# Kernel optimization log

Measured on AMD Instinct MI355X. Metric: run time of the kernel, lower is better.

## Reference

```python
import jax, jax.numpy as jnp
import numpy as np
import math

# Derived from BilateralDenoiser.set_influence(1.0):
#   sigma = max(2*influence, 1e-4) = 2.0; window N = 2*ceil(2.5*sigma)+1 = 11
SIGMA = 2.0
NORMAL_POWER = 128.0  # normal-similarity exponent in the CUDA kernel
EPS = 1e-4


def setup_inputs() -> dict:
    key = jax.random.key(0)
    k1, k2, k3 = jax.random.split(key, 3)
    B, H, W = 4, 1024, 1024
    col = jax.random.uniform(k1, (B, H, W, 3), jnp.float32)
    nrm = jax.random.normal(k2, (B, H, W, 3), jnp.float32)
    nrm = nrm / jnp.linalg.norm(nrm, axis=-1, keepdims=True)  # unit normals
    zdz = jax.random.uniform(k3, (B, H, W, 2), jnp.float32)   # (depth, |d depth|)
    return {"col": col, "nrm": nrm, "zdz": zdz}


def _denoise(col, nrm, zdz):
    # col/nrm: [B,H,W,3]; zdz: [B,H,W,2]
    B, H, W, _ = col.shape
    variance = SIGMA * SIGMA
    rad = int(math.ceil(SIGMA * 2.5))  # 5 -> 11x11 window
    yy = jnp.arange(H)
    xx = jnp.arange(W)
    c_z = zdz[..., 0]   # center depth
    c_dz = zdz[..., 1]  # center depth-gradient magnitude
    accum_c = jnp.zeros((B, H, W, 3), col.dtype)
    accum_w = jnp.zeros((B, H, W), col.dtype)
    for dy in range(-rad, rad + 1):
        my = (yy + dy >= 0) & (yy + dy < H)
        for dx in range(-rad, rad + 1):
            mx = (xx + dx >= 0) & (xx + dx < W)
            valid = (my[:, None] & mx[None, :]).astype(col.dtype)  # skip OOB taps
            # tap value at pixel (y+dy, x+dx), vectorized over the whole image
            t_col = jnp.roll(col, (-dy, -dx), axis=(1, 2))
            t_nrm = jnp.roll(nrm, (-dy, -dx), axis=(1, 2))
            t_z = jnp.roll(c_z, (-dy, -dx), axis=(1, 2))
            dist_sqr = float(dx * dx + dy * dy)
            dist = math.sqrt(dist_sqr)
            w_xy = math.exp(-dist_sqr / (2.0 * variance))  # spatial Gaussian (scalar)
            w_n = jnp.clip(jnp.sum(t_nrm * nrm, axis=-1), 0.0, 1.0) ** NORMAL_POWER
            w_d = jnp.exp(-jnp.abs(t_z - c_z) / jnp.maximum(c_dz * dist, EPS))
            w = w_xy * w_n * w_d * valid  # [B,H,W]
            accum_c = accum_c + t_col * w[..., None]
            accum_w = accum_w + w
    # module forward: col_w[..., 0:3] / col_w[..., 3:4]
    return accum_c / accum_w[..., None]


def reference(col, nrm, zdz):
    return _denoise(col, nrm, zdz)
```

## Files before the change

### kernel.cpp

```cpp
#include <hip/hip_runtime.h>

#define RAD 5
#define BX 32
#define BY 16
#define PX 2
#define NTX 16
#define TW (BX + 2*RAD)
#define TH (BY + 2*RAD)
#define TWP (TW + 1)

#define LOG2E 1.44269504f
#define CLAMP2 14426.950f
#define PC1 184.664963f
#define PC2 -92.3324814f
#define PC3 61.5549876f

__device__ __constant__ const float kLG[6] = {
    0.0f, -0.18033688f, -0.72134752f, -1.62303192f, -2.88539008f, -4.50842200f};
__device__ __constant__ const float kINVD[6][6] = {
    {1e30f,       1.0f,        0.5f,        0.33333333f, 0.25f,       0.2f},
    {1.0f,        0.70710678f, 0.44721360f, 0.31622777f, 0.24253563f, 0.19611614f},
    {0.5f,        0.44721360f, 0.35355339f, 0.27735010f, 0.22360680f, 0.18569534f},
    {0.33333333f, 0.31622777f, 0.27735010f, 0.23570226f, 0.2f,        0.17149859f},
    {0.25f,       0.24253563f, 0.22360680f, 0.2f,        0.17677670f, 0.15617376f},
    {0.2f,        0.19611614f, 0.18569534f, 0.17149859f, 0.15617376f, 0.14142136f}};

__global__ __launch_bounds__(256, 4) void bilateral_kernel(
    const float* __restrict__ col, const float* __restrict__ nrm,
    const float* __restrict__ zdz, float* __restrict__ out,
    int H, int W) {
  __shared__ float4 s_w[TH][TWP];
  __shared__ uint2  s_c[TH][TWP];

  const int bx = blockIdx.x, by = blockIdx.y, bz = blockIdx.z;
  const int gx0 = bx * BX - RAD;
  const int gy0 = by * BY - RAD;
  const int tid = threadIdx.x;
  const int plane = bz * H * W;

  for (int i = tid; i < TH * TW; i += 256) {
    const int r = i / TW;
    const int c = i - r * TW;
    const int gy = gy0 + r, gx = gx0 + c;
    float4 wv = make_float4(0.f, 0.f, 0.f, 0.f);
    uint2 cv = make_uint2(0u, 0u);
    if ((unsigned)gy < (unsigned)H && (unsigned)gx < (unsigned)W) {
      const int pix = plane + gy * W + gx;
      const float* np_ = nrm + pix * 3;
      wv.x = np_[0]; wv.y = np_[1]; wv.z = np_[2];
      wv.w = zdz[pix * 2];
      const float* cp = col + pix * 3;
      const unsigned ur = (__float_as_uint(cp[0]) + 0x8000u) >> 16;
      const unsigned ug = (__float_as_uint(cp[1]) + 0x8000u) & 0xffff0000u;
      const unsigned ub = (__float_as_uint(cp[2]) + 0x8000u) & 0xffff0000u;
      cv.x = ur | ug;
      cv.y = ub;
    }
    s_w[r][c] = wv;
    s_c[r][c] = cv;
  }
  __syncthreads();

  const int tx = tid & (NTX - 1);
  const int ty = tid >> 4;
  const int ly = ty + RAD;
  const int lxbase = tx * PX;
  const int oy = by * BY + ty;
  const int ox0 = bx * BX + tx * PX;

  float cnx[PX], cny[PX], cnz[PX], czv[PX], rc2[PX];
  float accx[PX], accy[PX], accz[PX], accw[PX];
#pragma unroll
  for (int p = 0; p < PX; ++p) {
    const float4 wv = s_w[ly][lxbase + RAD + p];
    cnx[p] = wv.x; cny[p] = wv.y; cnz[p] = wv.z;
    czv[p] = wv.w;
    const float cdz = zdz[(plane + oy * W + ox0 + p) * 2 + 1];
    rc2[p] = LOG2E / cdz;
    accx[p] = 0.f; accy[p] = 0.f; accz[p] = 0.f; accw[p] = 0.f;
  }

#pragma unroll 1
  for (int dy = -RAD; dy <= RAD; ++dy) {
    const int ady = dy < 0 ? -dy : dy;
    const float kg_ady = kLG[ady];
    const float* irow = kINVD[ady];
    float sA[6];
    float il2s[6][PX];
#pragma unroll
    for (int j = 0; j < 6; ++j) {
      sA[j] = kLG[j] + kg_ady;
      const float iv = irow[j];
#pragma unroll
      for (int p = 0; p < PX; ++p) il2s[j][p] = fminf(rc2[p] * iv, CLAMP2);
    }

    const float4* rowW = &s_w[ly + dy][lxbase];
    const uint2* rowC = &s_c[ly + dy][lxbase];

#pragma unroll
    for (int u = 0; u < 2 * RAD + PX; ++u) {
      const float4 wv = rowW[u];
      const uint2 cv = rowC[u];
      const float tr = __uint_as_float(cv.x << 16);
      const float tg = __uint_as_float(cv.x & 0xffff0000u);
      const float tb = __uint_as_float(cv.y);
#pragma unroll
      for (int p = 0; p < PX; ++p) {
        const int dx = u - RAD - p;
        if (dx < -RAD || dx > RAD) continue;
        const int adx = dx < 0 ? -dx : dx;
        const float d1 = fmaf(wv.x, cnx[p],
                         fmaf(wv.y, cny[p], fmaf(wv.z, cnz[p], -1.0f)));
        const float f = fmaxf(d1, -1.0f);
        const float dz = wv.w - czv[p];
        const float ct = fmaf(-fabsf(dz), il2s[adx][p], sA[adx]);
        const float t1 = fmaf(f, PC3, PC2);
        const float t2 = fmaf(f, t1, PC1);
        const float e = fmaf(f, t2, ct);
        const float w = __builtin_amdgcn_exp2f(e);
        accx[p] = fmaf(tr, w, accx[p]);
        accy[p] = fmaf(tg, w, accy[p]);
        accz[p] = fmaf(tb, w, accz[p]);
        accw[p] += w;
      }
    }
  }

#pragma unroll
  for (int p = 0; p < PX; ++p) {
    const int pix = plane + oy * W + ox0 + p;
    const float inv = 1.0f / accw[p];
    float* op = out + pix * 3;
    op[0] = accx[p] * inv;
    op[1] = accy[p] * inv;
    op[2] = accz[p] * inv;
  }
}

extern "C" void kernel_launch(void* const* d_in, const int* in_sizes, int n_in,
                              void* d_out, int out_size, void* d_ws, size_t ws_size,
                              hipStream_t stream) {
  const float* col = (const float*)d_in[0];
  const float* nrm = (const float*)d_in[1];
  const float* zdz = (const float*)d_in[2];
  float* out = (float*)d_out;
  const int H = 1024, W = 1024;
  const int B = in_sizes[0] / (3 * H * W);
  dim3 grid(W / BX, H / BY, B);
  bilateral_kernel<<<grid, dim3(256), 0, stream>>>(col, nrm, zdz, out, H, W);
}
```

Before: 316.3 us.

## Compute 2x2 outputs per thread with even/odd-split shared tile and larger blocks

Each thread now computes a 2x2 pixel patch instead of 1x2. Each loaded tap row feeds two output rows, which cuts shared-memory reads per tap. The shared tile is stored with even and odd columns split into halves, so adjacent threads read consecutive entries without padding and avoid bank conflicts. Blocks grow to 64x32 pixels with 512 threads, and the spatial-weight sums move to a precomputed 2D constant table with a sentinel row for out-of-range offsets. The cost is more registers per thread, which may reduce occupancy under the 512x4 launch bound.

```diff
diff --git a/kernel.cpp b/kernel.cpp
--- a/kernel.cpp
+++ b/kernel.cpp
@@ -1,13 +1,16 @@
 #include <hip/hip_runtime.h>
 
 #define RAD 5
-#define BX 32
-#define BY 16
+#define BX 64
+#define BY 32
 #define PX 2
-#define NTX 16
+#define PY 2
+#define NTX 32
+#define NTY 16
+#define NT 512
 #define TW (BX + 2*RAD)
 #define TH (BY + 2*RAD)
-#define TWP (TW + 1)
+#define HALF (TW/2)
 
 #define LOG2E 1.44269504f
 #define CLAMP2 14426.950f
@@ -15,22 +18,29 @@
 #define PC2 -92.3324814f
 #define PC3 61.5549876f
 
-__device__ __constant__ const float kLG[6] = {
-    0.0f, -0.18033688f, -0.72134752f, -1.62303192f, -2.88539008f, -4.50842200f};
-__device__ __constant__ const float kINVD[6][6] = {
+__device__ __constant__ const float kSA[7][6] = {
+    {0.0f, -0.18033688f, -0.72134752f, -1.62303192f, -2.88539008f, -4.50842200f},
+    {-0.18033688f, -0.36067376f, -0.90168440f, -1.80336880f, -3.06572696f, -4.68875888f},
+    {-0.72134752f, -0.90168440f, -1.44269504f, -2.34437944f, -3.60673760f, -5.22976952f},
+    {-1.62303192f, -1.80336880f, -2.34437944f, -3.24606384f, -4.50842200f, -6.13145392f},
+    {-2.88539008f, -3.06572696f, -3.60673760f, -4.50842200f, -5.77078016f, -7.39381208f},
+    {-4.50842200f, -4.68875888f, -5.22976952f, -6.13145392f, -7.39381208f, -9.01684400f},
+    {-1e30f, -1e30f, -1e30f, -1e30f, -1e30f, -1e30f}};
+__device__ __constant__ const float kINVD[7][6] = {
     {1e30f,       1.0f,        0.5f,        0.33333333f, 0.25f,       0.2f},
     {1.0f,        0.70710678f, 0.44721360f, 0.31622777f, 0.24253563f, 0.19611614f},
     {0.5f,        0.44721360f, 0.35355339f, 0.27735010f, 0.22360680f, 0.18569534f},
     {0.33333333f, 0.31622777f, 0.27735010f, 0.23570226f, 0.2f,        0.17149859f},
     {0.25f,       0.24253563f, 0.22360680f, 0.2f,        0.17677670f, 0.15617376f},
-    {0.2f,        0.19611614f, 0.18569534f, 0.17149859f, 0.15617376f, 0.14142136f}};
+    {0.2f,        0.19611614f, 0.18569534f, 0.17149859f, 0.15617376f, 0.14142136f},
+    {0.16666667f, 0.16439899f, 0.15811388f, 0.14907120f, 0.13867505f, 0.12803688f}};
 
-__global__ __launch_bounds__(256, 4) void bilateral_kernel(
+__global__ __launch_bounds__(512, 4) void bilateral_kernel(
     const float* __restrict__ col, const float* __restrict__ nrm,
     const float* __restrict__ zdz, float* __restrict__ out,
     int H, int W) {
-  __shared__ float4 s_w[TH][TWP];
-  __shared__ uint2  s_c[TH][TWP];
+  __shared__ float4 s_w[TH][TW];
+  __shared__ uint2  s_c[TH][TW];
 
   const int bx = blockIdx.x, by = blockIdx.y, bz = blockIdx.z;
   const int gx0 = bx * BX - RAD;
@@ -38,9 +48,10 @@
   const int tid = threadIdx.x;
   const int plane = bz * H * W;
 
-  for (int i = tid; i < TH * TW; i += 256) {
+  for (int i = tid; i < TH * TW; i += NT) {
     const int r = i / TW;
     const int c = i - r * TW;
+    const int pc = (c >> 1) + (c & 1) * HALF;
     const int gy = gy0 + r, gx = gx0 + c;
     float4 wv = make_float4(0.f, 0.f, 0.f, 0.f);
     uint2 cv = make_uint2(0u, 0u);
@@ -56,85 +67,114 @@
       cv.x = ur | ug;
       cv.y = ub;
     }
-    s_w[r][c] = wv;
-    s_c[r][c] = cv;
+    s_w[r][pc] = wv;
+    s_c[r][pc] = cv;
   }
   __syncthreads();
 
   const int tx = tid & (NTX - 1);
-  const int ty = tid >> 4;
-  const int ly = ty + RAD;
-  const int lxbase = tx * PX;
-  const int oy = by * BY + ty;
+  const int ty = tid >> 5;
+  const int oy0 = by * BY + ty * PY;
   const int ox0 = bx * BX + tx * PX;
 
-  float cnx[PX], cny[PX], cnz[PX], czv[PX], rc2[PX];
-  float accx[PX], accy[PX], accz[PX], accw[PX];
+  float cnx[2][2], cny[2][2], cnz[2][2], czv[2][2], rc2[2][2];
+  float accx[2][2], accy[2][2], accz[2][2], accw[2][2];
 #pragma unroll
-  for (int p = 0; p < PX; ++p) {
-    const float4 wv = s_w[ly][lxbase + RAD + p];
-    cnx[p] = wv.x; cny[p] = wv.y; cnz[p] = wv.z;
-    czv[p] = wv.w;
-    const float cdz = zdz[(plane + oy * W + ox0 + p) * 2 + 1];
-    rc2[p] = LOG2E / cdz;
-    accx[p] = 0.f; accy[p] = 0.f; accz[p] = 0.f; accw[p] = 0.f;
+  for (int q = 0; q < 2; ++q) {
+#pragma unroll
+    for (int p = 0; p < 2; ++p) {
+      const int c = tx * PX + RAD + p;
+      const int pc = (c >> 1) + (c & 1) * HALF;
+      const float4 wv = s_w[ty * PY + RAD + q][pc];
+      cnx[q][p] = wv.x; cny[q][p] = wv.y; cnz[q][p] = wv.z;
+      czv[q][p] = wv.w;
+      const float cdz = zdz[(plane + (oy0 + q) * W + ox0 + p) * 2 + 1];
+      rc2[q][p] = LOG2E / cdz;
+      accx[q][p] = 0.f; accy[q][p] = 0.f; accz[q][p] = 0.f; accw[q][p] = 0.f;
+    }
   }
 
 #pragma unroll 1
-  for (int dy = -RAD; dy <= RAD; ++dy) {
-    const int ady = dy < 0 ? -dy : dy;
-    const float kg_ady = kLG[ady];
-    const float* irow = kINVD[ady];
-    float sA[6];
-    float il2s[6][PX];
+  for (int trow = 0; trow < 2 * RAD + PY; ++trow) {
+    const int dy0 = trow - RAD;
+    const int ady0 = dy0 < 0 ? -dy0 : dy0;
+    const int dy1 = trow - RAD - 1;
+    const int ady1 = dy1 < 0 ? -dy1 : dy1;
+    const float* __restrict__ sa0 = kSA[ady0];
+    const float* __restrict__ sa1 = kSA[ady1];
+    const float* __restrict__ iv0 = kINVD[ady0];
+    const float* __restrict__ iv1 = kINVD[ady1];
+    float il20[6][2], il21[6][2];
 #pragma unroll
     for (int j = 0; j < 6; ++j) {
-      sA[j] = kLG[j] + kg_ady;
-      const float iv = irow[j];
+      const float v0 = iv0[j], v1 = iv1[j];
 #pragma unroll
-      for (int p = 0; p < PX; ++p) il2s[j][p] = fminf(rc2[p] * iv, CLAMP2);
+      for (int p = 0; p < 2; ++p) {
+        il20[j][p] = fminf(rc2[0][p] * v0, CLAMP2);
+        il21[j][p] = fminf(rc2[1][p] * v1, CLAMP2);
+      }
     }
-
-    const float4* rowW = &s_w[ly + dy][lxbase];
-    const uint2* rowC = &s_c[ly + dy][lxbase];
+    const float4* __restrict__ rowW = &s_w[ty * PY + trow][tx];
+    const uint2* __restrict__ rowC = &s_c[ty * PY + trow][tx];
 
 #pragma unroll
     for (int u = 0; u < 2 * RAD + PX; ++u) {
-      const float4 wv = rowW[u];
-      const uint2 cv = rowC[u];
-      const float tr = __uint_as_float(cv.x << 16);
-      const float tg = __uint_as_float(cv.x & 0xffff0000u);
-      const float tb = __uint_as_float(cv.y);
+      const int off = (u >> 1) + (u & 1) * HALF;
+      const float4 wv = rowW[off];
+      const uint2 cv = rowC[off];
+      const float tcr = __uint_as_float(cv.x << 16);
+      const float tcg = __uint_as_float(cv.x & 0xffff0000u);
+      const float tcb = __uint_as_float(cv.y);
 #pragma unroll
-      for (int p = 0; p < PX; ++p) {
+      for (int p = 0; p < 2; ++p) {
         const int dx = u - RAD - p;
         if (dx < -RAD || dx > RAD) continue;
         const int adx = dx < 0 ? -dx : dx;
-        const float d1 = fmaf(wv.x, cnx[p],
-                         fmaf(wv.y, cny[p], fmaf(wv.z, cnz[p], -1.0f)));
-        const float f = fmaxf(d1, -1.0f);
-        const float dz = wv.w - czv[p];
-        const float ct = fmaf(-fabsf(dz), il2s[adx][p], sA[adx]);
-        const float t1 = fmaf(f, PC3, PC2);
-        const float t2 = fmaf(f, t1, PC1);
-        const float e = fmaf(f, t2, ct);
-        const float w = __builtin_amdgcn_exp2f(e);
-        accx[p] = fmaf(tr, w, accx[p]);
-        accy[p] = fmaf(tg, w, accy[p]);
-        accz[p] = fmaf(tb, w, accz[p]);
-        accw[p] += w;
+        {
+          const float d1 = fmaf(wv.x, cnx[0][p],
+                           fmaf(wv.y, cny[0][p], fmaf(wv.z, cnz[0][p], -1.0f)));
+          const float f = fmaxf(d1, -1.0f);
+          const float dzv = wv.w - czv[0][p];
+          const float ct = fmaf(-fabsf(dzv), il20[adx][p], sa0[adx]);
+          const float t1 = fmaf(f, PC3, PC2);
+          const float t2 = fmaf(f, t1, PC1);
+          const float e = fmaf(f, t2, ct);
+          const float w = __builtin_amdgcn_exp2f(e);
+          accx[0][p] = fmaf(tcr, w, accx[0][p]);
+          accy[0][p] = fmaf(tcg, w, accy[0][p]);
+          accz[0][p] = fmaf(tcb, w, accz[0][p]);
+          accw[0][p] += w;
+        }
+        {
+          const float d1 = fmaf(wv.x, cnx[1][p],
+                           fmaf(wv.y, cny[1][p], fmaf(wv.z, cnz[1][p], -1.0f)));
+          const float f = fmaxf(d1, -1.0f);
+          const float dzv = wv.w - czv[1][p];
+          const float ct = fmaf(-fabsf(dzv), il21[adx][p], sa1[adx]);
+          const float t1 = fmaf(f, PC3, PC2);
+          const float t2 = fmaf(f, t1, PC1);
+          const float e = fmaf(f, t2, ct);
+          const float w = __builtin_amdgcn_exp2f(e);
+          accx[1][p] = fmaf(tcr, w, accx[1][p]);
+          accy[1][p] = fmaf(tcg, w, accy[1][p]);
+          accz[1][p] = fmaf(tcb, w, accz[1][p]);
+          accw[1][p] += w;
+        }
       }
     }
   }
 
 #pragma unroll
-  for (int p = 0; p < PX; ++p) {
-    const int pix = plane + oy * W + ox0 + p;
-    const float inv = 1.0f / accw[p];
-    float* op = out + pix * 3;
-    op[0] = accx[p] * inv;
-    op[1] = accy[p] * inv;
-    op[2] = accz[p] * inv;
+  for (int q = 0; q < 2; ++q) {
+#pragma unroll
+    for (int p = 0; p < 2; ++p) {
+      const int pix = plane + (oy0 + q) * W + ox0 + p;
+      const float inv = 1.0f / accw[q][p];
+      float* op = out + pix * 3;
+      op[0] = accx[q][p] * inv;
+      op[1] = accy[q][p] * inv;
+      op[2] = accz[q][p] * inv;
+    }
   }
 }
 
@@ -148,5 +188,5 @@
   const int H = 1024, W = 1024;
   const int B = in_sizes[0] / (3 * H * W);
   dim3 grid(W / BX, H / BY, B);
-  bilateral_kernel<<<grid, dim3(256), 0, stream>>>(col, nrm, zdz, out, H, W);
+  bilateral_kernel<<<grid, dim3(NT), 0, stream>>>(col, nrm, zdz, out, H, W);
 }
```

Result: slower. 349.9 us (+10.6%).
